# Performance work log

Measured on AMD Instinct MI355X. Metric: run time of the kernel, lower is better.

The kernel has to match this reference:

```python
import jax, jax.numpy as jnp
import numpy as np

DIM_MODEL = 2048
DQK = 64
DV = 64
NUM_HEADS = 32
NUM_GROUPS = 8
H_PER_G = NUM_HEADS // NUM_GROUPS
ROPE_THETA = 10000.0
RMS_EPS = 1e-6


def _rope(x):
    # x: [b, g, h, s, d]; rotate-half RoPE over last dim, positions along s.
    d = x.shape[-1]
    s = x.shape[-2]
    inv_freq = 1.0 / (ROPE_THETA ** (jnp.arange(0, d, 2, dtype=jnp.float32) / d))  # [d/2]
    ang = jnp.arange(s, dtype=jnp.float32)[:, None] * inv_freq[None, :]  # [s, d/2]
    cos, sin = jnp.cos(ang), jnp.sin(ang)
    x1, x2 = x[..., : d // 2], x[..., d // 2 :]
    return jnp.concatenate([x1 * cos - x2 * sin, x2 * cos + x1 * sin], axis=-1)


def setup_inputs() -> dict:
    key = jax.random.key(0)
    k1, k2, k3 = jax.random.split(key, 3)
    b, s = 2, 2048
    concat = NUM_HEADS * DQK + NUM_GROUPS * (DQK + DV)  # 3072
    x = jax.random.normal(k1, (b, s, DIM_MODEL), dtype=jnp.float32)
    w_in = jax.random.normal(k2, (concat, DIM_MODEL), dtype=jnp.float32) * (DIM_MODEL ** -0.5)
    w_out = jax.random.normal(k3, (DIM_MODEL, NUM_HEADS * DV), dtype=jnp.float32) * ((NUM_HEADS * DV) ** -0.5)
    rms_w = jnp.ones((DIM_MODEL,), dtype=jnp.float32)
    return {"x": x, "w_in": w_in, "w_out": w_out, "rms_w": rms_w}


def reference(x, w_in, w_out, rms_w):
    b, s, _ = x.shape
    # RMSNorm
    y = x * jax.lax.rsqrt(jnp.mean(x * x, axis=-1, keepdims=True) + RMS_EPS) * rms_w
    # In-projection (Linear, no bias): y @ w_in.T
    y = jnp.einsum('bsm,cm->bsc', y, w_in)
    cq = NUM_HEADS * DQK
    ck = NUM_GROUPS * DQK
    q, k, v = y[..., :cq], y[..., cq:cq + ck], y[..., cq + ck:]
    # q: b s (g h d) -> b g h s d ; k,v: b s (g d) -> b g 1 s d
    q = q.reshape(b, s, NUM_GROUPS, H_PER_G, DQK).transpose(0, 2, 3, 1, 4)
    k = k.reshape(b, s, NUM_GROUPS, DQK).transpose(0, 2, 1, 3)[:, :, None]
    v = v.reshape(b, s, NUM_GROUPS, DV).transpose(0, 2, 1, 3)[:, :, None]
    q = _rope(q)
    k = _rope(k)
    # scores with GQA broadcast over h
    qk = jnp.einsum('bghsd,bgxpd->bghsp', q, k) * (DQK ** -0.5)
    causal = jnp.tril(jnp.ones((s, s), dtype=bool))
    qk = jnp.where(causal, qk, -jnp.inf)
    attn = jax.nn.softmax(qk, axis=-1)
    o = jnp.einsum('bghsp,bgxpd->bghsd', attn, v)  # [b,g,h,s,d]
    o = o.transpose(0, 3, 1, 2, 4).reshape(b, s, NUM_HEADS * DV)
    y = jnp.einsum('bsc,mc->bsm', o, w_out)
    return x + y
```

## Files before the change

### kernel.cpp

```cpp
#include <hip/hip_runtime.h>
#include <hip/hip_bf16.h>

#define TOKENS   4096
#define SEQ      2048
#define DMODEL   2048
#define CONCAT   3072
#define NHEADS   32
#define NGROUPS  8
#define HPERG    4
#define CQ       2048
#define CK       512

typedef __attribute__((ext_vector_type(8))) short bf16x8;
typedef __attribute__((ext_vector_type(4))) float f32x4;

__device__ __forceinline__ ushort f2bf(float f) {
    __hip_bfloat16 h = __float2bfloat16(f);
    return __builtin_bit_cast(ushort, h);
}

#define GLOBAL_TO_LDS16(g, l)                                                  \
    __builtin_amdgcn_global_load_lds(                                          \
        (const __attribute__((address_space(1))) void*)(g),                    \
        (__attribute__((address_space(3))) void*)(l), 16, 0, 0)

__global__ void rmsnorm_kernel(const float* __restrict__ x,
                               const float* __restrict__ w,
                               ushort* __restrict__ y_bf) {
    int t = blockIdx.x;
    const float4* xr = (const float4*)(x + (size_t)t * DMODEL);
    float4 v[2];
    float ss = 0.f;
#pragma unroll
    for (int i = 0; i < 2; i++) {
        v[i] = xr[threadIdx.x + i * 256];
        ss += v[i].x * v[i].x + v[i].y * v[i].y + v[i].z * v[i].z + v[i].w * v[i].w;
    }
#pragma unroll
    for (int off = 32; off >= 1; off >>= 1) ss += __shfl_xor(ss, off);
    __shared__ float red[4];
    int wid = threadIdx.x >> 6;
    if ((threadIdx.x & 63) == 0) red[wid] = ss;
    __syncthreads();
    float total = red[0] + red[1] + red[2] + red[3];
    float scale = rsqrtf(total * (1.0f / DMODEL) + 1e-6f);
    const float4* wr = (const float4*)w;
    ushort4* yr = (ushort4*)(y_bf + (size_t)t * DMODEL);
#pragma unroll
    for (int i = 0; i < 2; i++) {
        int c = threadIdx.x + i * 256;
        float4 wv = wr[c];
        ushort4 o;
        o.x = f2bf(v[i].x * scale * wv.x);
        o.y = f2bf(v[i].y * scale * wv.y);
        o.z = f2bf(v[i].z * scale * wv.z);
        o.w = f2bf(v[i].w * scale * wv.w);
        yr[c] = o;
    }
}

__global__ void pack_bf16_kernel(const float* __restrict__ src,
                                 ushort* __restrict__ dst, int n4) {
    int i = blockIdx.x * 256 + threadIdx.x;
    if (i < n4) {
        float4 v = ((const float4*)src)[i];
        ushort4 o;
        o.x = f2bf(v.x); o.y = f2bf(v.y); o.z = f2bf(v.z); o.w = f2bf(v.w);
        ((ushort4*)dst)[i] = o;
    }
}

#define LGKM(nn) asm volatile("s_waitcnt lgkmcnt(" #nn ")" ::: "memory")
#define VMC(nn)  asm volatile("s_waitcnt vmcnt(" #nn ")" ::: "memory")
#define SBAR()   __builtin_amdgcn_s_barrier()
#define SCHED0() __builtin_amdgcn_sched_barrier(0)
#define PRIO(p)  __builtin_amdgcn_s_setprio(p)

#define RD_A(mh)                                                              \
    _Pragma("unroll") for (int mi = 0; mi < 4; mi++)                          \
    _Pragma("unroll") for (int ks = 0; ks < 2; ks++)                          \
        af[mi][ks] = *(const bf16x8*)(Ab +                                    \
            ((arow0 + (mh) * 64 + mi * 16) * 8 +                              \
             ((ks * 4 + quad) ^ an)) * 8);

#define RD_B(nh)                                                              \
    _Pragma("unroll") for (int ni = 0; ni < NFRAG; ni++)                      \
    _Pragma("unroll") for (int ks = 0; ks < 2; ks++)                          \
        bfr[nh][ni][ks] = *(const bf16x8*)(Bb +                               \
            ((brow0 + (nh) * (16 * NFRAG) + ni * 16) * 8 +                    \
             ((ks * 4 + quad) ^ an)) * 8);

#define MMQ(mh, nh)                                                           \
    _Pragma("unroll") for (int mi = 0; mi < 4; mi++)                          \
    _Pragma("unroll") for (int ni = 0; ni < NFRAG; ni++)                      \
    _Pragma("unroll") for (int ks = 0; ks < 2; ks++)                          \
        acc[(mh) * 4 + mi][(nh) * NFRAG + ni] =                               \
            __builtin_amdgcn_mfma_f32_16x16x32_bf16(af[mi][ks],               \
                bfr[nh][ni][ks], acc[(mh) * 4 + mi][(nh) * NFRAG + ni],       \
                0, 0, 0);

#define ISSUE_HALF(H_)                                                        \
    {                                                                         \
        int H = (H_);                                                         \
        if (H < 4 * NT) {                                                     \
            int t2 = H >> 2, j2 = H & 3;                                      \
            int k0 = t2 << 6;                                                 \
            if (j2 == 0 || j2 == 3) {                                         \
                int half = (j2 == 3);                                         \
                ushort* lb = (ushort*)&As[t2 & 1][0];                         \
                _Pragma("unroll") for (int c = 0; c < 2; c++) {               \
                    int s = w * 2 + c;                                        \
                    int row = (s >> 3) * 128 + half * 64 + (s & 7) * 8;       \
                    const ushort* g = Aptr +                                  \
                        (size_t)(bm + row + l8) * K + k0 + kb8;               \
                    GLOBAL_TO_LDS16(g, lb + row * 64);                        \
                }                                                             \
            } else {                                                          \
                int half = (j2 == 2);                                         \
                ushort* lb = (ushort*)&Bs[t2 & 1][0];                         \
                if constexpr (NFRAG == 2) {                                   \
                    _Pragma("unroll") for (int c = 0; c < 2; c++) {           \
                        int s = w * 2 + c;                                    \
                        int row = (s >> 2) * 64 + half * 32 + (s & 3) * 8;    \
                        const ushort* g = Bptr +                              \
                            (size_t)(bn + row + l8) * K + k0 + kb8;           \
                        GLOBAL_TO_LDS16(g, lb + row * 64);                    \
                    }                                                         \
                } else {                                                      \
                    int row = (w >> 1) * 32 + half * 16 + (w & 1) * 8;        \
                    const ushort* g = Bptr +                                  \
                        (size_t)(bn + row + l8) * K + k0 + kb8;               \
                    GLOBAL_TO_LDS16(g, lb + row * 64);                        \
                }                                                             \
            }                                                                 \
        }                                                                     \
    }

#define VMC_STEADY()                                                          \
    { if constexpr (NFRAG == 2) { VMC(6); } else { VMC(4); } }

#define TILE(t_, BUF)                                                         \
    {                                                                         \
        const ushort* Ab = &As[BUF][0];                                       \
        const ushort* Bb = &Bs[BUF][0];                                       \
                                                \
        RD_A(0); RD_B(0);                                                     \
        ISSUE_HALF(4 * (t_) + 7);                                             \
        LGKM(8);                                                              \
        SBAR(); LGKM(0); SCHED0();                                            \
        PRIO(1); MMQ(0, 0); PRIO(0);                                          \
        SBAR();                                                               \
                                                   \
        RD_B(1);                                                              \
        ISSUE_HALF(4 * (t_) + 8);                                             \
        SBAR(); LGKM(0); SCHED0();                                            \
        PRIO(1); MMQ(0, 1); PRIO(0);                                          \
        SBAR();                                                               \
                                                   \
        RD_A(1);                                                              \
        ISSUE_HALF(4 * (t_) + 9);                                             \
        SBAR(); LGKM(0); SCHED0();                                            \
        PRIO(1); MMQ(1, 0); PRIO(0);                                          \
        SBAR();                                                               \
                           \
        ISSUE_HALF(4 * (t_) + 10);                                            \
        SBAR(); SCHED0();                                                     \
        PRIO(1); MMQ(1, 1); PRIO(0);                                          \
        if ((t_) + 2 < NT)        { VMC_STEADY(); }                           \
        else if ((t_) + 2 == NT)  { VMC(0); }                                 \
        SBAR();                                                               \
    }

template <bool EPILOGUE, int NFRAG>
__global__ __launch_bounds__(512, 2) void gemm_nt_8ph(
        const ushort* __restrict__ Aptr, const ushort* __restrict__ Bptr,
        float* __restrict__ C, const float* __restrict__ X,
        float* __restrict__ OUT, int M, int N, int K) {
    __shared__ __align__(16) ushort As[2][256 * 64];
    __shared__ __align__(16) ushort Bs[2][NFRAG * 128 * 64];

    int nwg = (int)(gridDim.x * gridDim.y);
    int lin = (int)(blockIdx.y * gridDim.x + blockIdx.x);
    int swz = lin;
    if ((nwg & 7) == 0) swz = (lin & 7) * (nwg >> 3) + (lin >> 3);
    const int bm = (swz / (int)gridDim.x) * 256;
    const int bn = (swz % (int)gridDim.x) * (128 * NFRAG);

    const int w = threadIdx.x >> 6, lane = threadIdx.x & 63;
    const int n = lane & 15, quad = lane >> 4;
    const int wm = w >> 2, wn = w & 3;
    const int an = n & 7;
    const int l8 = lane >> 3;
    const int kb8 = ((lane & 7) ^ l8) * 8;
    const int arow0 = wm * 128 + n;
    const int brow0 = wn * (32 * NFRAG) + n;
    const int NT = K >> 6;

    f32x4 acc[8][2 * NFRAG] = {};
    bf16x8 af[4][2], bfr[2][NFRAG][2];

    ISSUE_HALF(0); ISSUE_HALF(1); ISSUE_HALF(2); ISSUE_HALF(3);
    ISSUE_HALF(4); ISSUE_HALF(5); ISSUE_HALF(6);
    VMC_STEADY();
    SBAR();

    for (int tt = 0; tt < NT; tt += 2) {
        TILE(tt, 0);
        TILE(tt + 1, 1);
    }

#pragma unroll
    for (int mi = 0; mi < 8; mi++)
#pragma unroll
        for (int ni = 0; ni < 2 * NFRAG; ni++) {
            int row = bm + wm * 128 + mi * 16 + quad * 4;
            int col = bn + wn * (32 * NFRAG) + ni * 16 + n;
#pragma unroll
            for (int r = 0; r < 4; r++) {
                size_t idx = (size_t)(row + r) * N + col;
                float v = acc[mi][ni][r];
                if (EPILOGUE) OUT[idx] = X[idx] + v;
                else          C[idx]   = v;
            }
        }
}

__global__ void pack_qkv_kernel(const float* __restrict__ qkv,
                                ushort* __restrict__ Qb,
                                ushort* __restrict__ Kb,
                                ushort* __restrict__ Vb) {
    __shared__ float cs[32], sn[32];
    __shared__ float tile[64][65];
    int tid = threadIdx.x;

    if (blockIdx.x < TOKENS) {
        int t = blockIdx.x;
        int b = t >> 11, s = t & (SEQ - 1);
        const float* row = qkv + (size_t)t * CONCAT;
        if (tid < 32) {
            const float LOG2_THETA = 13.287712379549449f;
            float inv = exp2f(-((float)tid / 32.0f) * LOG2_THETA);
            float ang = (float)s * inv;
            cs[tid] = cosf(ang);
            sn[tid] = sinf(ang);
        }
        __syncthreads();
        const float QSCALE = 0.18033688011112042f;
#pragma unroll
        for (int it = 0; it < (CQ + CK) / 2 / 256; it++) {
            int p = tid + it * 256;
            int head = p >> 5, j = p & 31;
            const float* hb = row + head * 64;
            float x1 = hb[j], x2 = hb[j + 32];
            float c = cs[j], s2 = sn[j];
            float o1 = x1 * c - x2 * s2;
            float o2 = x2 * c + x1 * s2;
            if (head < 32) {
                o1 *= QSCALE; o2 *= QSCALE;
                int g = head >> 2, h = head & 3;
                ushort* q = Qb + ((size_t)((b * 8 + g) * 4 + h) * SEQ + s) * 64;
                q[j]      = f2bf(o1);
                q[j + 32] = f2bf(o2);
            } else {
                int kh = head - 32;
                ushort* kk = Kb + ((size_t)(b * 8 + kh) * SEQ + s) * 64;
                kk[j]      = f2bf(o1);
                kk[j + 32] = f2bf(o2);
            }
        }
    } else {
        int bid = blockIdx.x - TOKENS;
        int st = bid & 31, bg = bid >> 5;
        int b = bg >> 3, g = bg & 7;
        int ls = tid >> 6;
        int d = tid & 63;
#pragma unroll
        for (int i = 0; i < 16; i++) {
            int s = st * 64 + i * 4 + ls;
            tile[i * 4 + ls][d] =
                qkv[(size_t)(b * SEQ + s) * CONCAT + CQ + CK + g * 64 + d];
        }
        __syncthreads();
#pragma unroll
        for (int i = 0; i < 16; i++) {
            int drow = i * 4 + ls;
            int scol = tid & 63;
            Vb[((size_t)(bg * 64 + drow)) * SEQ + st * 64 + scol] =
                f2bf(tile[scol][drow]);
        }
    }
}

#define AISSUE(kt_, buf_)                                                     \
    {                                                                         \
        const ushort* Kg_ = Kg0 + (kt_) * 64 * 64;                            \
        const ushort* Vg_ = Vg0 + (kt_) * 64;                                 \
        _Pragma("unroll") for (int r_ = 0; r_ < 2; r_++) {                    \
            GLOBAL_TO_LDS16(Kg_ + (r_ * 32 + w * 8) * 64 + koff,              \
                            &Kl[buf_][(r_ * 256 + w * 64) * 8]);              \
            GLOBAL_TO_LDS16(Vg_ + (size_t)(r_ * 32 + w * 8) * SEQ + voff,     \
                            &Vl[buf_][(r_ * 256 + w * 64) * 8]);              \
        }                                                                     \
    }

__global__ __launch_bounds__(256) void attn_mfma_kernel(
        const ushort* __restrict__ Qb, const ushort* __restrict__ Kb,
        const ushort* __restrict__ Vb, ushort* __restrict__ o_bf) {
    __shared__ __align__(16) ushort Kl[2][512 * 8];
    __shared__ __align__(16) ushort Vl[2][512 * 8];
    __shared__ __align__(16) uint   Pl[4][1056];

    int blk = blockIdx.x;
    int qt  = 15 - (blk >> 6);
    int bgh = blk & 63;
    int h = bgh & 3, g = (bgh >> 2) & 7, b = bgh >> 5;
    int w = threadIdx.x >> 6, lane = threadIdx.x & 63;
    int n = lane & 15, quad = lane >> 4;
    const int an = n & 7;
    int Q0 = qt * 128;
    int qw = Q0 + w * 32;

    const int l3 = lane >> 3;
    const int lx = (lane & 7) ^ l3;
    const int koff = l3 * 64 + lx * 8;
    const int voff = l3 * SEQ + lx * 8;

    const ushort* Qh  = Qb + (size_t)((b * 8 + g) * 4 + h) * (SEQ * 64);
    const ushort* Kg0 = Kb + (size_t)(b * 8 + g) * (SEQ * 64);
    const ushort* Vg0 = Vb + (size_t)(b * 8 + g) * (64 * SEQ);

    bf16x8 aq[2][2];
#pragma unroll
    for (int qg = 0; qg < 2; qg++)
#pragma unroll
        for (int ks = 0; ks < 2; ks++)
            aq[qg][ks] = *(const bf16x8*)(
                Qh + (size_t)(qw + qg * 16 + n) * 64 + ks * 32 + quad * 8);

    f32x4 od[2][4] = {};
    f32x4 od4[2] = {};

    short onev = (n == 0) ? (short)0x3F80 : (short)0;
    bf16x8 bones = {onev, onev, onev, onev, onev, onev, onev, onev};

    uint* Pw = Pl[w];
    int nkt = qt * 2 + 2;

    AISSUE(0, 0);
    AISSUE(1, 1);

    for (int kt = 0; kt < nkt; kt++) {
        int buf = kt & 1;
        if (kt + 1 < nkt) { VMC(4); } else { VMC(0); }
        SBAR(); SCHED0();

        bool act1 = (kt * 64 <= qw + 31);
        if (act1) {
            bool act0 = (kt * 64 <= qw + 15);
            const ushort* Kb_ = Kl[buf];
            const ushort* Vb_ = Vl[buf];

#pragma unroll
            for (int t16k = 0; t16k < 4; t16k++) {
                int krow = (t16k * 16 + n) * 8;
                bf16x8 kf0 = *(const bf16x8*)(Kb_ + (krow + (quad ^ an)) * 8);
                bf16x8 kf1 = *(const bf16x8*)(Kb_ + (krow + ((quad + 4) ^ an)) * 8);
                int key0 = kt * 64 + t16k * 16 + quad * 4;
#pragma unroll
                for (int qg = 0; qg < 2; qg++) {
                    if (qg == 0 && !act0) continue;
                    f32x4 c = {};
                    c = __builtin_amdgcn_mfma_f32_16x16x32_bf16(kf0, aq[qg][0], c, 0, 0, 0);
                    c = __builtin_amdgcn_mfma_f32_16x16x32_bf16(kf1, aq[qg][1], c, 0, 0, 0);
                    int qrow = qw + qg * 16 + n;
                    float p[4];
                    if (kt * 64 + 63 > qw + qg * 16) {
#pragma unroll
                        for (int r = 0; r < 4; r++)
                            p[r] = (key0 + r <= qrow) ? __builtin_amdgcn_exp2f(c[r]) : 0.f;
                    } else {
#pragma unroll
                        for (int r = 0; r < 4; r++)
                            p[r] = __builtin_amdgcn_exp2f(c[r]);
                    }
                    uint d0 = ((uint)f2bf(p[1]) << 16) | f2bf(p[0]);
                    uint d1 = ((uint)f2bf(p[3]) << 16) | f2bf(p[2]);
                    int base = ((t16k * 2 + (quad >> 1)) * 33 + qg * 16 + n) * 4
                               + (quad & 1) * 2;
                    Pw[base]     = d0;
                    Pw[base + 1] = d1;
                }
            }

#pragma unroll
            for (int kb2 = 0; kb2 < 2; kb2++) {
                int kb = kb2 * 4 + quad;
                bf16x8 bv[4];
#pragma unroll
                for (int dt = 0; dt < 4; dt++)
                    bv[dt] = *(const bf16x8*)(Vb_ +
                        (((dt * 16 + n) * 8 + (kb ^ an)) * 8));
#pragma unroll
                for (int qg = 0; qg < 2; qg++) {
                    if (qg == 0 && !act0) continue;
                    bf16x8 ap = *(const bf16x8*)(
                        (const ushort*)Pw + ((kb2 * 4 + quad) * 33 + qg * 16 + n) * 8);
#pragma unroll
                    for (int dt = 0; dt < 4; dt++)
                        od[qg][dt] = __builtin_amdgcn_mfma_f32_16x16x32_bf16(
                            ap, bv[dt], od[qg][dt], 0, 0, 0);
                    od4[qg] = __builtin_amdgcn_mfma_f32_16x16x32_bf16(
                        ap, bones, od4[qg], 0, 0, 0);
                }
            }
        }

        SCHED0(); SBAR();
        if (kt + 2 < nkt) AISSUE(kt + 2, buf);
    }

#pragma unroll
    for (int qg = 0; qg < 2; qg++) {
        float linv[4];
#pragma unroll
        for (int r = 0; r < 4; r++) {
            float lv = __shfl(od4[qg][r], lane & 48);
            linv[r] = __builtin_amdgcn_rcpf(lv);
        }
#pragma unroll
        for (int dt = 0; dt < 4; dt++)
#pragma unroll
            for (int r = 0; r < 4; r++) {
                int q = qw + qg * 16 + quad * 4 + r;
                int col = (g * 4 + h) * 64 + dt * 16 + n;
                o_bf[(size_t)(b * SEQ + q) * DMODEL + col] =
                    f2bf(od[qg][dt][r] * linv[r]);
            }
    }
}

extern "C" void kernel_launch(void* const* d_in, const int* in_sizes, int n_in,
                              void* d_out, int out_size, void* d_ws, size_t ws_size,
                              hipStream_t stream) {
    const float* x     = (const float*)d_in[0];
    const float* w_in  = (const float*)d_in[1];
    const float* w_out = (const float*)d_in[2];
    const float* rms_w = (const float*)d_in[3];
    float* out = (float*)d_out;

    const size_t MB = 1024 * 1024;
    char* ws = (char*)d_ws;
    float*  qkv      = (float*)ws;
    ushort* y_bf     = (ushort*)(ws + 48 * MB);
    ushort* w_in_bf  = (ushort*)(ws + 64 * MB);
    ushort* Qb       = (ushort*)(ws + 48 * MB);
    ushort* Kb       = (ushort*)(ws + 64 * MB);
    ushort* Vb       = (ushort*)(ws + 68 * MB);
    ushort* o_bf     = (ushort*)ws;
    ushort* w_out_bf = (ushort*)(ws + 16 * MB);

    rmsnorm_kernel<<<TOKENS, 256, 0, stream>>>(x, rms_w, y_bf);
    pack_bf16_kernel<<<(CONCAT * DMODEL / 4 + 255) / 256, 256, 0, stream>>>(
        w_in, w_in_bf, CONCAT * DMODEL / 4);

    gemm_nt_8ph<false, 2><<<dim3(CONCAT / 256, TOKENS / 256), 512, 0, stream>>>(
        y_bf, w_in_bf, qkv, nullptr, nullptr, TOKENS, CONCAT, DMODEL);

    pack_qkv_kernel<<<TOKENS + 512, 256, 0, stream>>>(
        qkv, Qb, Kb, Vb);
    pack_bf16_kernel<<<(DMODEL * DMODEL / 4 + 255) / 256, 256, 0, stream>>>(
        w_out, w_out_bf, DMODEL * DMODEL / 4);

    attn_mfma_kernel<<<1024, 256, 0, stream>>>(Qb, Kb, Vb, o_bf);

    gemm_nt_8ph<true, 1><<<dim3(DMODEL / 128, TOKENS / 256), 512, 0, stream>>>(
        o_bf, w_out_bf, nullptr, x, out, TOKENS, DMODEL, DMODEL);
}
```

Baseline: 300.9 us.

## Split attention block across 8 waves of 16 queries each with packed bf16 convert

The attention kernel moves from 4 waves of 32 queries each to 8 waves of 16 queries each (512 threads per block). The K/V tile loads are now spread over twice as many threads, so each thread issues one async load per tensor. The change also adds the packed v_cvt_pk_bf16_f32 conversion for P and s_setprio around the MFMA groups. It raises per-block parallelism and latency hiding at the cost of less K/V fragment reuse per wave and more barrier participants.

```diff
diff --git a/kernel.cpp b/kernel.cpp
--- a/kernel.cpp
+++ b/kernel.cpp
@@ -17,6 +17,12 @@
 __device__ __forceinline__ ushort f2bf(float f) {
     __hip_bfloat16 h = __float2bfloat16(f);
     return __builtin_bit_cast(ushort, h);
+}
+
+__device__ __forceinline__ uint cvt_pk_bf16(float lo, float hi) {
+    uint r;
+    asm("v_cvt_pk_bf16_f32 %0, %1, %2" : "=v"(r) : "v"(lo), "v"(hi));
+    return r;
 }
 
 #define GLOBAL_TO_LDS16(g, l)                                                  \
@@ -295,20 +301,18 @@
     {                                                                         \
         const ushort* Kg_ = Kg0 + (kt_) * 64 * 64;                            \
         const ushort* Vg_ = Vg0 + (kt_) * 64;                                 \
-        _Pragma("unroll") for (int r_ = 0; r_ < 2; r_++) {                    \
-            GLOBAL_TO_LDS16(Kg_ + (r_ * 32 + w * 8) * 64 + koff,              \
-                            &Kl[buf_][(r_ * 256 + w * 64) * 8]);              \
-            GLOBAL_TO_LDS16(Vg_ + (size_t)(r_ * 32 + w * 8) * SEQ + voff,     \
-                            &Vl[buf_][(r_ * 256 + w * 64) * 8]);              \
-        }                                                                     \
-    }
-
-__global__ __launch_bounds__(256) void attn_mfma_kernel(
+        GLOBAL_TO_LDS16(Kg_ + (w * 8 + l3) * 64 + lx * 8,                     \
+                        &Kl[buf_][(size_t)threadIdx.x * 8]);                  \
+        GLOBAL_TO_LDS16(Vg_ + (size_t)(w * 8 + l3) * SEQ + lx * 8,            \
+                        &Vl[buf_][(size_t)threadIdx.x * 8]);                  \
+    }
+
+__global__ __launch_bounds__(512) void attn_mfma_kernel(
         const ushort* __restrict__ Qb, const ushort* __restrict__ Kb,
         const ushort* __restrict__ Vb, ushort* __restrict__ o_bf) {
     __shared__ __align__(16) ushort Kl[2][512 * 8];
     __shared__ __align__(16) ushort Vl[2][512 * 8];
-    __shared__ __align__(16) uint   Pl[4][1056];
+    __shared__ __align__(16) uint   Pl[8][544];
 
     int blk = blockIdx.x;
     int qt  = 15 - (blk >> 6);
@@ -318,27 +322,23 @@
     int n = lane & 15, quad = lane >> 4;
     const int an = n & 7;
     int Q0 = qt * 128;
-    int qw = Q0 + w * 32;
+    int qw = Q0 + w * 16;
 
     const int l3 = lane >> 3;
     const int lx = (lane & 7) ^ l3;
-    const int koff = l3 * 64 + lx * 8;
-    const int voff = l3 * SEQ + lx * 8;
 
     const ushort* Qh  = Qb + (size_t)((b * 8 + g) * 4 + h) * (SEQ * 64);
     const ushort* Kg0 = Kb + (size_t)(b * 8 + g) * (SEQ * 64);
     const ushort* Vg0 = Vb + (size_t)(b * 8 + g) * (64 * SEQ);
 
-    bf16x8 aq[2][2];
-#pragma unroll
-    for (int qg = 0; qg < 2; qg++)
-#pragma unroll
-        for (int ks = 0; ks < 2; ks++)
-            aq[qg][ks] = *(const bf16x8*)(
-                Qh + (size_t)(qw + qg * 16 + n) * 64 + ks * 32 + quad * 8);
-
-    f32x4 od[2][4] = {};
-    f32x4 od4[2] = {};
+    bf16x8 aq[2];
+#pragma unroll
+    for (int ks = 0; ks < 2; ks++)
+        aq[ks] = *(const bf16x8*)(
+            Qh + (size_t)(qw + n) * 64 + ks * 32 + quad * 8);
+
+    f32x4 od[4] = {};
+    f32x4 od4 = {};
 
     short onev = (n == 0) ? (short)0x3F80 : (short)0;
     bf16x8 bones = {onev, onev, onev, onev, onev, onev, onev, onev};
@@ -351,12 +351,11 @@
 
     for (int kt = 0; kt < nkt; kt++) {
         int buf = kt & 1;
-        if (kt + 1 < nkt) { VMC(4); } else { VMC(0); }
+        if (kt + 1 < nkt) { VMC(2); } else { VMC(0); }
         SBAR(); SCHED0();
 
-        bool act1 = (kt * 64 <= qw + 31);
-        if (act1) {
-            bool act0 = (kt * 64 <= qw + 15);
+        bool act = (kt * 64 <= qw + 15);
+        if (act) {
             const ushort* Kb_ = Kl[buf];
             const ushort* Vb_ = Vl[buf];
 
@@ -366,30 +365,28 @@
                 bf16x8 kf0 = *(const bf16x8*)(Kb_ + (krow + (quad ^ an)) * 8);
                 bf16x8 kf1 = *(const bf16x8*)(Kb_ + (krow + ((quad + 4) ^ an)) * 8);
                 int key0 = kt * 64 + t16k * 16 + quad * 4;
-#pragma unroll
-                for (int qg = 0; qg < 2; qg++) {
-                    if (qg == 0 && !act0) continue;
-                    f32x4 c = {};
-                    c = __builtin_amdgcn_mfma_f32_16x16x32_bf16(kf0, aq[qg][0], c, 0, 0, 0);
-                    c = __builtin_amdgcn_mfma_f32_16x16x32_bf16(kf1, aq[qg][1], c, 0, 0, 0);
-                    int qrow = qw + qg * 16 + n;
-                    float p[4];
-                    if (kt * 64 + 63 > qw + qg * 16) {
-#pragma unroll
-                        for (int r = 0; r < 4; r++)
-                            p[r] = (key0 + r <= qrow) ? __builtin_amdgcn_exp2f(c[r]) : 0.f;
-                    } else {
-#pragma unroll
-                        for (int r = 0; r < 4; r++)
-                            p[r] = __builtin_amdgcn_exp2f(c[r]);
-                    }
-                    uint d0 = ((uint)f2bf(p[1]) << 16) | f2bf(p[0]);
-                    uint d1 = ((uint)f2bf(p[3]) << 16) | f2bf(p[2]);
-                    int base = ((t16k * 2 + (quad >> 1)) * 33 + qg * 16 + n) * 4
-                               + (quad & 1) * 2;
-                    Pw[base]     = d0;
-                    Pw[base + 1] = d1;
+                f32x4 c = {};
+                PRIO(1);
+                c = __builtin_amdgcn_mfma_f32_16x16x32_bf16(kf0, aq[0], c, 0, 0, 0);
+                c = __builtin_amdgcn_mfma_f32_16x16x32_bf16(kf1, aq[1], c, 0, 0, 0);
+                PRIO(0);
+                int qrow = qw + n;
+                float p[4];
+                if (kt * 64 + 63 > qw) {
+#pragma unroll
+                    for (int r = 0; r < 4; r++)
+                        p[r] = (key0 + r <= qrow) ? __builtin_amdgcn_exp2f(c[r]) : 0.f;
+                } else {
+#pragma unroll
+                    for (int r = 0; r < 4; r++)
+                        p[r] = __builtin_amdgcn_exp2f(c[r]);
                 }
+                uint d0 = cvt_pk_bf16(p[0], p[1]);
+                uint d1 = cvt_pk_bf16(p[2], p[3]);
+                int base = ((t16k * 2 + (quad >> 1)) * 17 + n) * 4
+                           + (quad & 1) * 2;
+                Pw[base]     = d0;
+                Pw[base + 1] = d1;
             }
 
 #pragma unroll
@@ -400,18 +397,16 @@
                 for (int dt = 0; dt < 4; dt++)
                     bv[dt] = *(const bf16x8*)(Vb_ +
                         (((dt * 16 + n) * 8 + (kb ^ an)) * 8));
-#pragma unroll
-                for (int qg = 0; qg < 2; qg++) {
-                    if (qg == 0 && !act0) continue;
-                    bf16x8 ap = *(const bf16x8*)(
-                        (const ushort*)Pw + ((kb2 * 4 + quad) * 33 + qg * 16 + n) * 8);
-#pragma unroll
-                    for (int dt = 0; dt < 4; dt++)
-                        od[qg][dt] = __builtin_amdgcn_mfma_f32_16x16x32_bf16(
-                            ap, bv[dt], od[qg][dt], 0, 0, 0);
-                    od4[qg] = __builtin_amdgcn_mfma_f32_16x16x32_bf16(
-                        ap, bones, od4[qg], 0, 0, 0);
-                }
+                bf16x8 ap = *(const bf16x8*)(
+                    (const ushort*)Pw + ((kb2 * 4 + quad) * 17 + n) * 8);
+                PRIO(1);
+#pragma unroll
+                for (int dt = 0; dt < 4; dt++)
+                    od[dt] = __builtin_amdgcn_mfma_f32_16x16x32_bf16(
+                        ap, bv[dt], od[dt], 0, 0, 0);
+                od4 = __builtin_amdgcn_mfma_f32_16x16x32_bf16(
+                    ap, bones, od4, 0, 0, 0);
+                PRIO(0);
             }
         }
 
@@ -419,24 +414,21 @@
         if (kt + 2 < nkt) AISSUE(kt + 2, buf);
     }
 
-#pragma unroll
-    for (int qg = 0; qg < 2; qg++) {
-        float linv[4];
+    float linv[4];
+#pragma unroll
+    for (int r = 0; r < 4; r++) {
+        float lv = __shfl(od4[r], lane & 48);
+        linv[r] = __builtin_amdgcn_rcpf(lv);
+    }
+#pragma unroll
+    for (int dt = 0; dt < 4; dt++)
 #pragma unroll
         for (int r = 0; r < 4; r++) {
-            float lv = __shfl(od4[qg][r], lane & 48);
-            linv[r] = __builtin_amdgcn_rcpf(lv);
-        }
-#pragma unroll
-        for (int dt = 0; dt < 4; dt++)
-#pragma unroll
-            for (int r = 0; r < 4; r++) {
-                int q = qw + qg * 16 + quad * 4 + r;
-                int col = (g * 4 + h) * 64 + dt * 16 + n;
-                o_bf[(size_t)(b * SEQ + q) * DMODEL + col] =
-                    f2bf(od[qg][dt][r] * linv[r]);
-            }
-    }
+            int q = qw + quad * 4 + r;
+            int col = (g * 4 + h) * 64 + dt * 16 + n;
+            o_bf[(size_t)(b * SEQ + q) * DMODEL + col] =
+                f2bf(od[dt][r] * linv[r]);
+        }
 }
 
 extern "C" void kernel_launch(void* const* d_in, const int* in_sizes, int n_in,
@@ -471,7 +463,7 @@
     pack_bf16_kernel<<<(DMODEL * DMODEL / 4 + 255) / 256, 256, 0, stream>>>(
         w_out, w_out_bf, DMODEL * DMODEL / 4);
 
-    attn_mfma_kernel<<<1024, 256, 0, stream>>>(Qb, Kb, Vb, o_bf);
+    attn_mfma_kernel<<<1024, 512, 0, stream>>>(Qb, Kb, Vb, o_bf);
 
     gemm_nt_8ph<true, 1><<<dim3(DMODEL / 128, TOKENS / 256), 512, 0, stream>>>(
         o_bf, w_out_bf, nullptr, x, out, TOKENS, DMODEL, DMODEL);
```

After: 290.5 us. 3.4% less time.
